# Kernel tuning notes

Measured on AMD Instinct MI355X. Metric: run time of the kernel, lower is better.

Reference implementation:

```python
import jax, jax.numpy as jnp
import numpy as np

B, H, D, V = 1024, 4, 256, 100000


def setup_inputs() -> dict:
    key = jax.random.key(0)
    k1, k2, k3, k4 = jax.random.split(key, 4)
    x = jax.random.normal(k1, (B, D), dtype=jnp.float32)
    # Glorot-normal-ish scaling for the learned matrices
    proj_mat = jax.random.normal(k2, (H * D, D), dtype=jnp.float32) * (2.0 / (H * D + D)) ** 0.5
    mix_mat = jax.random.normal(k3, (H, D), dtype=jnp.float32) * (2.0 / (H + D)) ** 0.5
    emb = jax.random.normal(k4, (V, D), dtype=jnp.float32) * 0.05
    return {"x": x, "proj_mat": proj_mat, "mix_mat": mix_mat, "emb": emb}


def reference(x, proj_mat, mix_mat, emb):
    # per-head projection: [B, H*D] -> [B, H, D]
    proj = jnp.tanh(x @ proj_mat.T).reshape(B, H, D)
    # mixture weights over heads: [B, H]
    pi = jax.nn.softmax(x @ mix_mat.T, axis=-1)
    # full-vocab logits per head: [B, H, V]
    head_logits = jnp.einsum("bhd,vd->bhv", proj, emb)
    head_probs = jax.nn.softmax(head_logits, axis=-1)
    # weighted mixture over heads -> [B, V]
    probs = jnp.einsum("bh,bhv->bv", pi, head_probs)
    return probs
```

## Files before the change

kernel.cpp:

```cpp
#include <hip/hip_runtime.h>
#include <stdint.h>


#define VOCAB 100000
#define NVB 391
#define VPAD 100096

typedef __attribute__((ext_vector_type(8))) short short8;
typedef __attribute__((ext_vector_type(4))) float f32x4;

__device__ __forceinline__ short f2bf(float f) {
  uint32_t u = __float_as_uint(f);
  u = (u + 0x7FFFu + ((u >> 16) & 1u)) >> 16;
  return (short)u;
}

#define VMCNT(n) asm volatile("s_waitcnt vmcnt(" #n ")" ::: "memory")
#define LGKM0()  asm volatile("s_waitcnt lgkmcnt(0)" ::: "memory")
#define SCHED0() __builtin_amdgcn_sched_barrier(0)
#define BAR()    __builtin_amdgcn_s_barrier()

__global__ __launch_bounds__(256) void proj_kernel(const float* __restrict__ x,
                                                   const float* __restrict__ pm,
                                                   short* __restrict__ projA) {
  __shared__ float xs[64][36];
  __shared__ float ps[64][36];
  const int tid = threadIdx.x;
  const int tx = tid & 15, ty = tid >> 4;
  const int m0 = blockIdx.y * 64, n0 = blockIdx.x * 64;
  float acc[4][4];
#pragma unroll
  for (int i = 0; i < 4; i++)
#pragma unroll
    for (int j = 0; j < 4; j++) acc[i][j] = 0.f;

  for (int k0 = 0; k0 < 256; k0 += 32) {
    const int r = tid >> 2, c = (tid & 3) * 8;
    *(float4*)&xs[r][c]     = *(const float4*)&x[(m0 + r) * 256 + k0 + c];
    *(float4*)&xs[r][c + 4] = *(const float4*)&x[(m0 + r) * 256 + k0 + c + 4];
    *(float4*)&ps[r][c]     = *(const float4*)&pm[(n0 + r) * 256 + k0 + c];
    *(float4*)&ps[r][c + 4] = *(const float4*)&pm[(n0 + r) * 256 + k0 + c + 4];
    __syncthreads();
#pragma unroll
    for (int kk = 0; kk < 32; kk += 4) {
      float4 xa[4], pb[4];
#pragma unroll
      for (int i = 0; i < 4; i++) xa[i] = *(const float4*)&xs[ty * 4 + i][kk];
#pragma unroll
      for (int j = 0; j < 4; j++) pb[j] = *(const float4*)&ps[tx * 4 + j][kk];
#pragma unroll
      for (int i = 0; i < 4; i++)
#pragma unroll
        for (int j = 0; j < 4; j++)
          acc[i][j] += xa[i].x * pb[j].x + xa[i].y * pb[j].y +
                       xa[i].z * pb[j].z + xa[i].w * pb[j].w;
    }
    __syncthreads();
  }
#pragma unroll
  for (int i = 0; i < 4; i++)
#pragma unroll
    for (int j = 0; j < 4; j++)
      projA[(size_t)(m0 + ty * 4 + i) * 1024 + (n0 + tx * 4 + j)] = f2bf(tanhf(acc[i][j]));
}

__global__ __launch_bounds__(256) void pi_kernel(const float* __restrict__ x,
                                                 const float* __restrict__ mm,
                                                 float* __restrict__ pi) {
  int b = blockIdx.x * 256 + threadIdx.x;
  if (b >= 1024) return;
  float acc[4] = {0.f, 0.f, 0.f, 0.f};
  for (int k = 0; k < 256; k += 4) {
    float4 xv = *(const float4*)&x[(size_t)b * 256 + k];
#pragma unroll
    for (int h = 0; h < 4; h++) {
      float4 mv = *(const float4*)&mm[h * 256 + k];
      acc[h] += xv.x * mv.x + xv.y * mv.y + xv.z * mv.z + xv.w * mv.w;
    }
  }
  float mx = fmaxf(fmaxf(acc[0], acc[1]), fmaxf(acc[2], acc[3]));
  float e[4], ssum = 0.f;
#pragma unroll
  for (int h = 0; h < 4; h++) { e[h] = __expf(acc[h] - mx); ssum += e[h]; }
#pragma unroll
  for (int h = 0; h < 4; h++) pi[b * 4 + h] = e[h] / ssum;
}

__global__ __launch_bounds__(256) void embB_kernel(const float* __restrict__ emb,
                                                   short* __restrict__ embB) {
  size_t i = ((size_t)blockIdx.x * 256 + threadIdx.x) * 8;
  size_t row = i >> 8;
  short8 b8;
  if (row < VOCAB) {
    float4 f0 = *(const float4*)&emb[i];
    float4 f1 = *(const float4*)&emb[i + 4];
    b8[0] = f2bf(f0.x); b8[1] = f2bf(f0.y); b8[2] = f2bf(f0.z); b8[3] = f2bf(f0.w);
    b8[4] = f2bf(f1.x); b8[5] = f2bf(f1.y); b8[6] = f2bf(f1.z); b8[7] = f2bf(f1.w);
  } else {
#pragma unroll
    for (int j = 0; j < 8; ++j) b8[j] = 0;
  }
  *(short8*)&embB[i] = b8;
}


__device__ __forceinline__ void stage_AB(const char* gA, const char* gB, char* sm,
                                         int buf, int kt, int wid) {
#pragma unroll
  for (int h = 0; h < 2; ++h)
#pragma unroll
    for (int j = 0; j < 2; ++j) {
      __builtin_amdgcn_global_load_lds(
          (const __attribute__((address_space(1))) void*)(gA + kt * 128 + h * 65536 + j * 32768),
          (__attribute__((address_space(3))) void*)(sm + buf * 65536 + h * 16384 + j * 8192 + wid * 1024),
          16, 0, 0);
      __builtin_amdgcn_global_load_lds(
          (const __attribute__((address_space(1))) void*)(gB + kt * 128 + h * 65536 + j * 32768),
          (__attribute__((address_space(3))) void*)(sm + buf * 65536 + 32768 + h * 16384 + j * 8192 + wid * 1024),
          16, 0, 0);
    }
}

template <int KT>
__device__ __forceinline__ void k_step(char* sm, const char* gA, const char* gB, int wid,
                                       f32x4 (&acc)[8][4], int aK0, int aK1, int bK0, int bK1) {
  constexpr int CB = (KT & 1) * 65536;
  if (KT < 3) {
    stage_AB(gA, gB, sm, (KT + 1) & 1, KT + 1, wid);
    SCHED0();
    VMCNT(8);
  } else {
    SCHED0();
    VMCNT(0);
  }
  BAR();
  SCHED0();

  short8 b[4][2], a0[4][2], a1[4][2];
#pragma unroll
  for (int j = 0; j < 4; ++j) {
    b[j][0] = *(const short8*)(sm + CB + bK0 + j * 2048);
    b[j][1] = *(const short8*)(sm + CB + bK1 + j * 2048);
  }
#pragma unroll
  for (int i = 0; i < 4; ++i) {
    a0[i][0] = *(const short8*)(sm + CB + aK0 + i * 2048);
    a0[i][1] = *(const short8*)(sm + CB + aK1 + i * 2048);
  }
  __builtin_amdgcn_s_setprio(1);
#pragma unroll
  for (int ks = 0; ks < 2; ++ks)
#pragma unroll
    for (int i = 0; i < 4; ++i)
#pragma unroll
      for (int j = 0; j < 4; ++j)
        acc[i][j] = __builtin_amdgcn_mfma_f32_16x16x32_bf16(a0[i][ks], b[j][ks], acc[i][j], 0, 0, 0);
  __builtin_amdgcn_s_setprio(0);
#pragma unroll
  for (int i = 0; i < 4; ++i) {
    a1[i][0] = *(const short8*)(sm + CB + aK0 + (4 + i) * 2048);
    a1[i][1] = *(const short8*)(sm + CB + aK1 + (4 + i) * 2048);
  }
  LGKM0();
  SCHED0();
  BAR();
  SCHED0();
  __builtin_amdgcn_s_setprio(1);
#pragma unroll
  for (int ks = 0; ks < 2; ++ks)
#pragma unroll
    for (int i = 0; i < 4; ++i)
#pragma unroll
      for (int j = 0; j < 4; ++j)
        acc[4 + i][j] =
            __builtin_amdgcn_mfma_f32_16x16x32_bf16(a1[i][ks], b[j][ks], acc[4 + i][j], 0, 0, 0);
  __builtin_amdgcn_s_setprio(0);
}

template <int MODE>
__global__ __launch_bounds__(512, 2) void mos_gemm8(const short* __restrict__ projA_s,
                                                    const short* __restrict__ embB_s,
                                                    const float* __restrict__ w,
                                                    float* __restrict__ part,
                                                    float* __restrict__ out) {
  __shared__ __align__(16) char sm[131072];
  const int tid = threadIdx.x;
  const int lane = tid & 63, wid = tid >> 6;
  const int wr = wid >> 2, wc = wid & 3;
  const int l15 = lane & 15, l4 = lane >> 4;

  const int id = blockIdx.x;
  const int sw = (id & 7) * 782 + (id >> 3);
  const int vb = sw >> 4, mb = sw & 15;
  const int m0 = mb * 256;
  const int v0 = vb * 256;

  const int cxor = ((tid & 7) ^ ((tid >> 3) & 7)) * 16;
  const char* gA = (const char*)projA_s + (size_t)(m0 + (tid >> 3)) * 512 + cxor;
  const char* gB = (const char*)embB_s + (size_t)(v0 + (tid >> 3)) * 512 + cxor;

  const int sA = l15 & 7;
  const int aK0 = (wr * 128 + l15) * 128 + ((l4 ^ sA) << 4);
  const int aK1 = (wr * 128 + l15) * 128 + (((4 + l4) ^ sA) << 4);
  const int bK0 = 32768 + (wc * 64 + l15) * 128 + ((l4 ^ sA) << 4);
  const int bK1 = 32768 + (wc * 64 + l15) * 128 + (((4 + l4) ^ sA) << 4);

  f32x4 acc[8][4];
#pragma unroll
  for (int i = 0; i < 8; ++i)
#pragma unroll
    for (int j = 0; j < 4; ++j) acc[i][j] = (f32x4){0.f, 0.f, 0.f, 0.f};

  stage_AB(gA, gB, sm, 0, 0, wid);
  SCHED0();

  k_step<0>(sm, gA, gB, wid, acc, aK0, aK1, bK0, bK1);
  k_step<1>(sm, gA, gB, wid, acc, aK0, aK1, bK0, bK1);
  k_step<2>(sm, gA, gB, wid, acc, aK0, aK1, bK0, bK1);
  k_step<3>(sm, gA, gB, wid, acc, aK0, aK1, bK0, bK1);

  if (MODE == 0) {
#pragma unroll
    for (int mi = 0; mi < 8; ++mi) {
      float p[4] = {0.f, 0.f, 0.f, 0.f};
#pragma unroll
      for (int ni = 0; ni < 4; ++ni) {
        int v = v0 + wc * 64 + ni * 16 + l15;
        bool ok = v < VOCAB;
#pragma unroll
        for (int r = 0; r < 4; ++r) {
          float e = __expf(acc[mi][ni][r]);
          p[r] += ok ? e : 0.f;
        }
      }
#pragma unroll
      for (int r = 0; r < 4; ++r) {
        p[r] += __shfl_xor(p[r], 1, 64);
        p[r] += __shfl_xor(p[r], 2, 64);
        p[r] += __shfl_xor(p[r], 4, 64);
        p[r] += __shfl_xor(p[r], 8, 64);
      }
      if (l15 == 0) {
        float4 pv = {p[0], p[1], p[2], p[3]};
        *(float4*)(sm + (wc * 256 + wr * 128 + mi * 16 + l4 * 4) * 4) = pv;
      }
    }
    __syncthreads();
    if (tid < 256) {
      const float* rf = (const float*)sm;
      float ssum = rf[tid] + rf[256 + tid] + rf[512 + tid] + rf[768 + tid];
      part[(size_t)vb * 4096 + m0 + tid] = ssum;
    }
  } else {
#pragma unroll
    for (int mi = 0; mi < 8; ++mi) {
      int mbase = m0 + wr * 128 + mi * 16;
      float4 wv = *(const float4*)&w[mbase + l4 * 4];
      size_t brow = (size_t)(mbase >> 2) + l4;
#pragma unroll
      for (int ni = 0; ni < 4; ++ni) {
        int v = v0 + wc * 64 + ni * 16 + l15;
        float val = wv.x * __expf(acc[mi][ni][0]) + wv.y * __expf(acc[mi][ni][1]) +
                    wv.z * __expf(acc[mi][ni][2]) + wv.w * __expf(acc[mi][ni][3]);
        if (v < VOCAB) out[brow * VOCAB + v] = val;
      }
    }
  }
}

__global__ __launch_bounds__(256) void reduce_w(const float* __restrict__ part,
                                                const float* __restrict__ pi,
                                                float* __restrict__ w) {
  int m = blockIdx.x * 256 + threadIdx.x;
  float sum = 0.f;
  for (int c = 0; c < NVB; ++c) sum += part[(size_t)c * 4096 + m];
  w[m] = pi[m] / sum;
}

extern "C" void kernel_launch(void* const* d_in, const int* in_sizes, int n_in,
                              void* d_out, int out_size, void* d_ws, size_t ws_size,
                              hipStream_t stream) {
  const float* x        = (const float*)d_in[0];
  const float* proj_mat = (const float*)d_in[1];
  const float* mix_mat  = (const float*)d_in[2];
  const float* emb      = (const float*)d_in[3];
  float* out = (float*)d_out;

  char* ws = (char*)d_ws;
  short* projA = (short*)ws;
  float* pi    = (float*)(ws + (2u << 20));
  float* w     = (float*)(ws + (2u << 20) + 16384);
  short* embB  = (short*)(ws + (4u << 20));
  float* part  = (float*)(ws + (4u << 20) + (size_t)VPAD * 512);

  dim3 g1(16, 16);
  proj_kernel<<<g1, 256, 0, stream>>>(x, proj_mat, projA);
  pi_kernel<<<4, 256, 0, stream>>>(x, mix_mat, pi);
  embB_kernel<<<VPAD / 8, 256, 0, stream>>>(emb, embB);

  mos_gemm8<0><<<16 * NVB, 512, 0, stream>>>(projA, embB, nullptr, part, nullptr);
  reduce_w<<<16, 256, 0, stream>>>(part, pi, w);
  mos_gemm8<1><<<16 * NVB, 512, 0, stream>>>(projA, embB, w, nullptr, out);
}
```

Measured before the change: 688.0 us.

## Split k-step into quarter MFMA phases interleaved with staged global-to-LDS loads

Restructures each K step of the bf16 GEMM into four MFMA quadrants, issuing next-tile A and B global_load_lds pieces between them with finer-grained vmcnt waits and barriers. The goal is to overlap memory staging with compute instead of front-loading all loads per step. It also folds log2(e) into the bf16 embedding conversion so the epilogues can use exp2f instead of __expf, saving a multiply per exponential. The extra barriers and the finer wait bookkeeping add synchronization overhead and raise the risk of ordering errors.

```diff
diff --git a/kernel.cpp b/kernel.cpp
--- a/kernel.cpp
+++ b/kernel.cpp
@@ -90,12 +90,13 @@
                                                    short* __restrict__ embB) {
   size_t i = ((size_t)blockIdx.x * 256 + threadIdx.x) * 8;
   size_t row = i >> 8;
+  const float C = 1.44269504088896f;
   short8 b8;
   if (row < VOCAB) {
     float4 f0 = *(const float4*)&emb[i];
     float4 f1 = *(const float4*)&emb[i + 4];
-    b8[0] = f2bf(f0.x); b8[1] = f2bf(f0.y); b8[2] = f2bf(f0.z); b8[3] = f2bf(f0.w);
-    b8[4] = f2bf(f1.x); b8[5] = f2bf(f1.y); b8[6] = f2bf(f1.z); b8[7] = f2bf(f1.w);
+    b8[0] = f2bf(f0.x * C); b8[1] = f2bf(f0.y * C); b8[2] = f2bf(f0.z * C); b8[3] = f2bf(f0.w * C);
+    b8[4] = f2bf(f1.x * C); b8[5] = f2bf(f1.y * C); b8[6] = f2bf(f1.z * C); b8[7] = f2bf(f1.w * C);
   } else {
 #pragma unroll
     for (int j = 0; j < 8; ++j) b8[j] = 0;
@@ -104,77 +105,91 @@
 }
 
 
-__device__ __forceinline__ void stage_AB(const char* gA, const char* gB, char* sm,
-                                         int buf, int kt, int wid) {
-#pragma unroll
-  for (int h = 0; h < 2; ++h)
-#pragma unroll
-    for (int j = 0; j < 2; ++j) {
-      __builtin_amdgcn_global_load_lds(
-          (const __attribute__((address_space(1))) void*)(gA + kt * 128 + h * 65536 + j * 32768),
-          (__attribute__((address_space(3))) void*)(sm + buf * 65536 + h * 16384 + j * 8192 + wid * 1024),
-          16, 0, 0);
-      __builtin_amdgcn_global_load_lds(
-          (const __attribute__((address_space(1))) void*)(gB + kt * 128 + h * 65536 + j * 32768),
-          (__attribute__((address_space(3))) void*)(sm + buf * 65536 + 32768 + h * 16384 + j * 8192 + wid * 1024),
-          16, 0, 0);
-    }
-}
+#define MFMA_Q(AF, BF, MOFF, NOFF)                                                        \
+  __builtin_amdgcn_s_setprio(1);                                                          \
+  _Pragma("unroll") for (int ks = 0; ks < 2; ++ks)                                        \
+      _Pragma("unroll") for (int qi = 0; qi < 4; ++qi)                                    \
+          _Pragma("unroll") for (int qj = 0; qj < 2; ++qj)                                \
+              acc[(MOFF) + qi][(NOFF) + qj] = __builtin_amdgcn_mfma_f32_16x16x32_bf16(    \
+                  AF[qi][ks], BF[qj][ks], acc[(MOFF) + qi][(NOFF) + qj], 0, 0, 0);        \
+  __builtin_amdgcn_s_setprio(0);
 
 template <int KT>
 __device__ __forceinline__ void k_step(char* sm, const char* gA, const char* gB, int wid,
                                        f32x4 (&acc)[8][4], int aK0, int aK1, int bK0, int bK1) {
-  constexpr int CB = (KT & 1) * 65536;
-  if (KT < 3) {
-    stage_AB(gA, gB, sm, (KT + 1) & 1, KT + 1, wid);
-    SCHED0();
-    VMCNT(8);
-  } else {
-    SCHED0();
-    VMCNT(0);
-  }
-  BAR();
-  SCHED0();
-
-  short8 b[4][2], a0[4][2], a1[4][2];
-#pragma unroll
-  for (int j = 0; j < 4; ++j) {
-    b[j][0] = *(const short8*)(sm + CB + bK0 + j * 2048);
-    b[j][1] = *(const short8*)(sm + CB + bK1 + j * 2048);
+  const int CB = (KT & 1) * 65536;
+  char* NB = sm + ((KT + 1) & 1) * 65536;
+  short8 a0[4][2], a1[4][2], b0[2][2], b1[2][2];
+
+#pragma unroll
+  for (int j = 0; j < 2; ++j) {
+    b0[j][0] = *(const short8*)(sm + CB + bK0 + j * 2048);
+    b0[j][1] = *(const short8*)(sm + CB + bK1 + j * 2048);
   }
 #pragma unroll
   for (int i = 0; i < 4; ++i) {
     a0[i][0] = *(const short8*)(sm + CB + aK0 + i * 2048);
     a0[i][1] = *(const short8*)(sm + CB + aK1 + i * 2048);
   }
-  __builtin_amdgcn_s_setprio(1);
-#pragma unroll
-  for (int ks = 0; ks < 2; ++ks)
-#pragma unroll
-    for (int i = 0; i < 4; ++i)
-#pragma unroll
-      for (int j = 0; j < 4; ++j)
-        acc[i][j] = __builtin_amdgcn_mfma_f32_16x16x32_bf16(a0[i][ks], b[j][ks], acc[i][j], 0, 0, 0);
-  __builtin_amdgcn_s_setprio(0);
+  if constexpr (KT < 3) {
+#pragma unroll
+    for (int h = 0; h < 2; ++h)
+      __builtin_amdgcn_global_load_lds(
+          (const __attribute__((address_space(1))) void*)(gA + (KT + 1) * 128 + h * 65536),
+          (__attribute__((address_space(3))) void*)(NB + h * 16384 + wid * 1024), 16, 0, 0);
+  }
+  SCHED0();
+  BAR();
+  LGKM0();
+  SCHED0();
+  MFMA_Q(a0, b0, 0, 0);
+  BAR();
+
+#pragma unroll
+  for (int j = 0; j < 2; ++j) {
+    b1[j][0] = *(const short8*)(sm + CB + bK0 + (2 + j) * 2048);
+    b1[j][1] = *(const short8*)(sm + CB + bK1 + (2 + j) * 2048);
+  }
+  if constexpr (KT < 3) {
+#pragma unroll
+    for (int h = 0; h < 2; ++h)
+#pragma unroll
+      for (int j = 0; j < 2; ++j)
+        __builtin_amdgcn_global_load_lds(
+            (const __attribute__((address_space(1))) void*)(gB + (KT + 1) * 128 + h * 65536 + j * 32768),
+            (__attribute__((address_space(3))) void*)(NB + 32768 + h * 16384 + j * 8192 + wid * 1024),
+            16, 0, 0);
+  }
+  SCHED0();
+  BAR();
+  LGKM0();
+  SCHED0();
+  MFMA_Q(a0, b1, 0, 2);
+  if constexpr (KT < 3) { VMCNT(6); } else { VMCNT(0); }
+  BAR();
+
 #pragma unroll
   for (int i = 0; i < 4; ++i) {
     a1[i][0] = *(const short8*)(sm + CB + aK0 + (4 + i) * 2048);
     a1[i][1] = *(const short8*)(sm + CB + aK1 + (4 + i) * 2048);
   }
+  if constexpr (KT < 3) {
+#pragma unroll
+    for (int h = 0; h < 2; ++h)
+      __builtin_amdgcn_global_load_lds(
+          (const __attribute__((address_space(1))) void*)(gA + (KT + 1) * 128 + h * 65536 + 32768),
+          (__attribute__((address_space(3))) void*)(NB + h * 16384 + 8192 + wid * 1024), 16, 0, 0);
+  }
+  SCHED0();
+  BAR();
   LGKM0();
   SCHED0();
-  BAR();
-  SCHED0();
-  __builtin_amdgcn_s_setprio(1);
-#pragma unroll
-  for (int ks = 0; ks < 2; ++ks)
-#pragma unroll
-    for (int i = 0; i < 4; ++i)
-#pragma unroll
-      for (int j = 0; j < 4; ++j)
-        acc[4 + i][j] =
-            __builtin_amdgcn_mfma_f32_16x16x32_bf16(a1[i][ks], b[j][ks], acc[4 + i][j], 0, 0, 0);
-  __builtin_amdgcn_s_setprio(0);
+  MFMA_Q(a1, b1, 4, 2);
+  BAR();
+
+  MFMA_Q(a1, b0, 4, 0);
+  if constexpr (KT < 3) { VMCNT(2); }
+  BAR();
 }
 
 template <int MODE>
@@ -211,8 +226,27 @@
 #pragma unroll
     for (int j = 0; j < 4; ++j) acc[i][j] = (f32x4){0.f, 0.f, 0.f, 0.f};
 
-  stage_AB(gA, gB, sm, 0, 0, wid);
-  SCHED0();
+#pragma unroll
+  for (int h = 0; h < 2; ++h)
+    __builtin_amdgcn_global_load_lds(
+        (const __attribute__((address_space(1))) void*)(gA + h * 65536),
+        (__attribute__((address_space(3))) void*)(sm + h * 16384 + wid * 1024), 16, 0, 0);
+#pragma unroll
+  for (int h = 0; h < 2; ++h)
+#pragma unroll
+    for (int j = 0; j < 2; ++j)
+      __builtin_amdgcn_global_load_lds(
+          (const __attribute__((address_space(1))) void*)(gB + h * 65536 + j * 32768),
+          (__attribute__((address_space(3))) void*)(sm + 32768 + h * 16384 + j * 8192 + wid * 1024),
+          16, 0, 0);
+#pragma unroll
+  for (int h = 0; h < 2; ++h)
+    __builtin_amdgcn_global_load_lds(
+        (const __attribute__((address_space(1))) void*)(gA + h * 65536 + 32768),
+        (__attribute__((address_space(3))) void*)(sm + h * 16384 + 8192 + wid * 1024), 16, 0, 0);
+  SCHED0();
+  VMCNT(2);
+  BAR();
 
   k_step<0>(sm, gA, gB, wid, acc, aK0, aK1, bK0, bK1);
   k_step<1>(sm, gA, gB, wid, acc, aK0, aK1, bK0, bK1);
@@ -229,7 +263,7 @@
         bool ok = v < VOCAB;
 #pragma unroll
         for (int r = 0; r < 4; ++r) {
-          float e = __expf(acc[mi][ni][r]);
+          float e = exp2f(acc[mi][ni][r]);
           p[r] += ok ? e : 0.f;
         }
       }
@@ -260,8 +294,8 @@
 #pragma unroll
       for (int ni = 0; ni < 4; ++ni) {
         int v = v0 + wc * 64 + ni * 16 + l15;
-        float val = wv.x * __expf(acc[mi][ni][0]) + wv.y * __expf(acc[mi][ni][1]) +
-                    wv.z * __expf(acc[mi][ni][2]) + wv.w * __expf(acc[mi][ni][3]);
+        float val = wv.x * exp2f(acc[mi][ni][0]) + wv.y * exp2f(acc[mi][ni][1]) +
+                    wv.z * exp2f(acc[mi][ni][2]) + wv.w * exp2f(acc[mi][ni][3]);
         if (v < VOCAB) out[brow * VOCAB + v] = val;
       }
     }
```

New measurement: 724.6 us. 5.3% more time.

## Keep embedding tile in registers and stream projection rows through LDS

Applied to the files above, without the earlier changes.

Restructures both GEMM passes so each 256-thread block keeps a 128-row embedding slice resident in registers across the full K=256. It then loops over 512 M rows in 64-row sub-tiles staged through a small double-buffered LDS, with the epilogue run per sub-tile. Per-strip partial sums go straight to global memory, which doubles the strip count that reduce_w sums. Out-of-range vocab stores are sent to a dump buffer instead of masked. The log2(e) factor is folded into the bf16 embedding conversion so exp2f replaces __expf. The goal is less LDS traffic and better overlap, at the cost of heavy register pressure and more partial-sum traffic.

```diff
diff --git a/kernel.cpp b/kernel.cpp
--- a/kernel.cpp
+++ b/kernel.cpp
@@ -3,7 +3,8 @@
 
 
 #define VOCAB 100000
-#define NVB 391
+#define NVB 782
+#define NSTRIPS 1564
 #define VPAD 100096
 
 typedef __attribute__((ext_vector_type(8))) short short8;
@@ -90,12 +91,13 @@
                                                    short* __restrict__ embB) {
   size_t i = ((size_t)blockIdx.x * 256 + threadIdx.x) * 8;
   size_t row = i >> 8;
+  const float C = 1.44269504088896f;
   short8 b8;
   if (row < VOCAB) {
     float4 f0 = *(const float4*)&emb[i];
     float4 f1 = *(const float4*)&emb[i + 4];
-    b8[0] = f2bf(f0.x); b8[1] = f2bf(f0.y); b8[2] = f2bf(f0.z); b8[3] = f2bf(f0.w);
-    b8[4] = f2bf(f1.x); b8[5] = f2bf(f1.y); b8[6] = f2bf(f1.z); b8[7] = f2bf(f1.w);
+    b8[0] = f2bf(f0.x * C); b8[1] = f2bf(f0.y * C); b8[2] = f2bf(f0.z * C); b8[3] = f2bf(f0.w * C);
+    b8[4] = f2bf(f1.x * C); b8[5] = f2bf(f1.y * C); b8[6] = f2bf(f1.z * C); b8[7] = f2bf(f1.w * C);
   } else {
 #pragma unroll
     for (int j = 0; j < 8; ++j) b8[j] = 0;
@@ -104,124 +106,70 @@
 }
 
 
-__device__ __forceinline__ void stage_AB(const char* gA, const char* gB, char* sm,
-                                         int buf, int kt, int wid) {
-#pragma unroll
-  for (int h = 0; h < 2; ++h)
-#pragma unroll
-    for (int j = 0; j < 2; ++j) {
+template <int VM, bool DO_STAGE, int KH>
+__device__ __forceinline__ void k_step(char* sm, const char* gA0, int sOff, int wid,
+                                       const int (&aadr)[4], const short8 (&Bf)[4][8],
+                                       f32x4 (&acc)[2][4]) {
+  constexpr int buf = KH;
+  if constexpr (DO_STAGE) {
+#pragma unroll
+    for (int j = 0; j < 4; ++j)
       __builtin_amdgcn_global_load_lds(
-          (const __attribute__((address_space(1))) void*)(gA + kt * 128 + h * 65536 + j * 32768),
-          (__attribute__((address_space(3))) void*)(sm + buf * 65536 + h * 16384 + j * 8192 + wid * 1024),
+          (const __attribute__((address_space(1))) void*)(gA0 + sOff + j * 8192),
+          (__attribute__((address_space(3))) void*)(sm + (buf ^ 1) * 16384 + j * 4096 + wid * 1024),
           16, 0, 0);
-      __builtin_amdgcn_global_load_lds(
-          (const __attribute__((address_space(1))) void*)(gB + kt * 128 + h * 65536 + j * 32768),
-          (__attribute__((address_space(3))) void*)(sm + buf * 65536 + 32768 + h * 16384 + j * 8192 + wid * 1024),
-          16, 0, 0);
-    }
-}
-
-template <int KT>
-__device__ __forceinline__ void k_step(char* sm, const char* gA, const char* gB, int wid,
-                                       f32x4 (&acc)[8][4], int aK0, int aK1, int bK0, int bK1) {
-  constexpr int CB = (KT & 1) * 65536;
-  if (KT < 3) {
-    stage_AB(gA, gB, sm, (KT + 1) & 1, KT + 1, wid);
-    SCHED0();
-    VMCNT(8);
-  } else {
-    SCHED0();
-    VMCNT(0);
-  }
+  }
+  SCHED0();
+  if constexpr (VM == 12)      { VMCNT(12); }
+  else if constexpr (VM == 6)  { VMCNT(6); }
+  else if constexpr (VM == 4)  { VMCNT(4); }
+  else                         { VMCNT(0); }
   BAR();
-  SCHED0();
-
-  short8 b[4][2], a0[4][2], a1[4][2];
-#pragma unroll
-  for (int j = 0; j < 4; ++j) {
-    b[j][0] = *(const short8*)(sm + CB + bK0 + j * 2048);
-    b[j][1] = *(const short8*)(sm + CB + bK1 + j * 2048);
-  }
-#pragma unroll
-  for (int i = 0; i < 4; ++i) {
-    a0[i][0] = *(const short8*)(sm + CB + aK0 + i * 2048);
-    a0[i][1] = *(const short8*)(sm + CB + aK1 + i * 2048);
-  }
+  short8 a[2][4];
+#pragma unroll
+  for (int mi = 0; mi < 2; ++mi)
+#pragma unroll
+    for (int ks = 0; ks < 2; ++ks)
+      a[mi][ks] = *(const short8*)(sm + buf * 16384 + mi * 4096 + aadr[ks]);
   __builtin_amdgcn_s_setprio(1);
 #pragma unroll
   for (int ks = 0; ks < 2; ++ks)
 #pragma unroll
-    for (int i = 0; i < 4; ++i)
-#pragma unroll
-      for (int j = 0; j < 4; ++j)
-        acc[i][j] = __builtin_amdgcn_mfma_f32_16x16x32_bf16(a0[i][ks], b[j][ks], acc[i][j], 0, 0, 0);
+    for (int mi = 0; mi < 2; ++mi)
+#pragma unroll
+      for (int ni = 0; ni < 4; ++ni)
+        acc[mi][ni] = __builtin_amdgcn_mfma_f32_16x16x32_bf16(a[mi][ks], Bf[ni][KH * 4 + ks],
+                                                              acc[mi][ni], 0, 0, 0);
   __builtin_amdgcn_s_setprio(0);
 #pragma unroll
-  for (int i = 0; i < 4; ++i) {
-    a1[i][0] = *(const short8*)(sm + CB + aK0 + (4 + i) * 2048);
-    a1[i][1] = *(const short8*)(sm + CB + aK1 + (4 + i) * 2048);
-  }
+  for (int mi = 0; mi < 2; ++mi)
+#pragma unroll
+    for (int ks = 2; ks < 4; ++ks)
+      a[mi][ks] = *(const short8*)(sm + buf * 16384 + mi * 4096 + aadr[ks]);
   LGKM0();
   SCHED0();
   BAR();
-  SCHED0();
   __builtin_amdgcn_s_setprio(1);
 #pragma unroll
-  for (int ks = 0; ks < 2; ++ks)
-#pragma unroll
-    for (int i = 0; i < 4; ++i)
-#pragma unroll
-      for (int j = 0; j < 4; ++j)
-        acc[4 + i][j] =
-            __builtin_amdgcn_mfma_f32_16x16x32_bf16(a1[i][ks], b[j][ks], acc[4 + i][j], 0, 0, 0);
+  for (int ks = 2; ks < 4; ++ks)
+#pragma unroll
+    for (int mi = 0; mi < 2; ++mi)
+#pragma unroll
+      for (int ni = 0; ni < 4; ++ni)
+        acc[mi][ni] = __builtin_amdgcn_mfma_f32_16x16x32_bf16(a[mi][ks], Bf[ni][KH * 4 + ks],
+                                                              acc[mi][ni], 0, 0, 0);
   __builtin_amdgcn_s_setprio(0);
 }
 
 template <int MODE>
-__global__ __launch_bounds__(512, 2) void mos_gemm8(const short* __restrict__ projA_s,
-                                                    const short* __restrict__ embB_s,
-                                                    const float* __restrict__ w,
-                                                    float* __restrict__ part,
-                                                    float* __restrict__ out) {
-  __shared__ __align__(16) char sm[131072];
-  const int tid = threadIdx.x;
-  const int lane = tid & 63, wid = tid >> 6;
-  const int wr = wid >> 2, wc = wid & 3;
-  const int l15 = lane & 15, l4 = lane >> 4;
-
-  const int id = blockIdx.x;
-  const int sw = (id & 7) * 782 + (id >> 3);
-  const int vb = sw >> 4, mb = sw & 15;
-  const int m0 = mb * 256;
-  const int v0 = vb * 256;
-
-  const int cxor = ((tid & 7) ^ ((tid >> 3) & 7)) * 16;
-  const char* gA = (const char*)projA_s + (size_t)(m0 + (tid >> 3)) * 512 + cxor;
-  const char* gB = (const char*)embB_s + (size_t)(v0 + (tid >> 3)) * 512 + cxor;
-
-  const int sA = l15 & 7;
-  const int aK0 = (wr * 128 + l15) * 128 + ((l4 ^ sA) << 4);
-  const int aK1 = (wr * 128 + l15) * 128 + (((4 + l4) ^ sA) << 4);
-  const int bK0 = 32768 + (wc * 64 + l15) * 128 + ((l4 ^ sA) << 4);
-  const int bK1 = 32768 + (wc * 64 + l15) * 128 + (((4 + l4) ^ sA) << 4);
-
-  f32x4 acc[8][4];
-#pragma unroll
-  for (int i = 0; i < 8; ++i)
-#pragma unroll
-    for (int j = 0; j < 4; ++j) acc[i][j] = (f32x4){0.f, 0.f, 0.f, 0.f};
-
-  stage_AB(gA, gB, sm, 0, 0, wid);
-  SCHED0();
-
-  k_step<0>(sm, gA, gB, wid, acc, aK0, aK1, bK0, bK1);
-  k_step<1>(sm, gA, gB, wid, acc, aK0, aK1, bK0, bK1);
-  k_step<2>(sm, gA, gB, wid, acc, aK0, aK1, bK0, bK1);
-  k_step<3>(sm, gA, gB, wid, acc, aK0, aK1, bK0, bK1);
-
+__device__ __forceinline__ void epilogue(int mt, int m0, int v0, int vb, int wr, int wc,
+                                         int l15, int l4, int tid, int bid,
+                                         const float* __restrict__ w, float* __restrict__ part,
+                                         float* __restrict__ dump, float* __restrict__ out,
+                                         f32x4 (&acc)[2][4]) {
   if (MODE == 0) {
 #pragma unroll
-    for (int mi = 0; mi < 8; ++mi) {
+    for (int mi = 0; mi < 2; ++mi) {
       float p[4] = {0.f, 0.f, 0.f, 0.f};
 #pragma unroll
       for (int ni = 0; ni < 4; ++ni) {
@@ -229,7 +177,7 @@
         bool ok = v < VOCAB;
 #pragma unroll
         for (int r = 0; r < 4; ++r) {
-          float e = __expf(acc[mi][ni][r]);
+          float e = exp2f(acc[mi][ni][r]);
           p[r] += ok ? e : 0.f;
         }
       }
@@ -241,31 +189,94 @@
         p[r] += __shfl_xor(p[r], 8, 64);
       }
       if (l15 == 0) {
+        int m = m0 + mt * 64 + wr * 32 + mi * 16 + l4 * 4;
         float4 pv = {p[0], p[1], p[2], p[3]};
-        *(float4*)(sm + (wc * 256 + wr * 128 + mi * 16 + l4 * 4) * 4) = pv;
+        *(float4*)(part + (size_t)(vb * 2 + wc) * 4096 + m) = pv;
       }
     }
-    __syncthreads();
-    if (tid < 256) {
-      const float* rf = (const float*)sm;
-      float ssum = rf[tid] + rf[256 + tid] + rf[512 + tid] + rf[768 + tid];
-      part[(size_t)vb * 4096 + m0 + tid] = ssum;
-    }
   } else {
 #pragma unroll
-    for (int mi = 0; mi < 8; ++mi) {
-      int mbase = m0 + wr * 128 + mi * 16;
+    for (int mi = 0; mi < 2; ++mi) {
+      int mbase = m0 + mt * 64 + wr * 32 + mi * 16;
       float4 wv = *(const float4*)&w[mbase + l4 * 4];
       size_t brow = (size_t)(mbase >> 2) + l4;
 #pragma unroll
       for (int ni = 0; ni < 4; ++ni) {
         int v = v0 + wc * 64 + ni * 16 + l15;
-        float val = wv.x * __expf(acc[mi][ni][0]) + wv.y * __expf(acc[mi][ni][1]) +
-                    wv.z * __expf(acc[mi][ni][2]) + wv.w * __expf(acc[mi][ni][3]);
-        if (v < VOCAB) out[brow * VOCAB + v] = val;
+        float val = wv.x * exp2f(acc[mi][ni][0]) + wv.y * exp2f(acc[mi][ni][1]) +
+                    wv.z * exp2f(acc[mi][ni][2]) + wv.w * exp2f(acc[mi][ni][3]);
+        float* tgt = (v < VOCAB) ? (out + brow * VOCAB + v)
+                                 : (dump + ((bid & 255) * 256 + tid));
+        *tgt = val;
       }
     }
   }
+#pragma unroll
+  for (int mi = 0; mi < 2; ++mi)
+#pragma unroll
+    for (int ni = 0; ni < 4; ++ni) acc[mi][ni] = (f32x4){0.f, 0.f, 0.f, 0.f};
+}
+
+template <int MODE>
+__global__ __launch_bounds__(256, 2) void mos_gemm(const short* __restrict__ projA_s,
+                                                   const short* __restrict__ embB_s,
+                                                   const float* __restrict__ w,
+                                                   float* __restrict__ part,
+                                                   float* __restrict__ dump,
+                                                   float* __restrict__ out) {
+  __shared__ __align__(16) char sm[32768];
+  const int tid = threadIdx.x;
+  const int lane = tid & 63, wid = tid >> 6;
+  const int wr = wid >> 1, wc = wid & 1;
+  const int l15 = lane & 15, l4 = lane >> 4;
+  const int bid = blockIdx.x;
+
+  const int sw = (bid & 7) * 782 + (bid >> 3);
+  const int vb = sw >> 3, me = sw & 7;
+  const int v0 = vb * 128, m0 = me * 512;
+
+  const char* gA0 = (const char*)projA_s + (size_t)(m0 + (tid >> 4)) * 512 +
+                    (((tid & 15) ^ ((tid >> 4) & 7)) << 4);
+  int aadr[4];
+#pragma unroll
+  for (int ks = 0; ks < 4; ++ks)
+    aadr[ks] = wr * 8192 + l15 * 256 + ((((ks * 4) + l4) ^ (l15 & 7)) << 4);
+
+#pragma unroll
+  for (int j = 0; j < 4; ++j)
+    __builtin_amdgcn_global_load_lds(
+        (const __attribute__((address_space(1))) void*)(gA0 + j * 8192),
+        (__attribute__((address_space(3))) void*)(sm + j * 4096 + wid * 1024), 16, 0, 0);
+  SCHED0();
+
+  short8 Bf[4][8];
+  {
+    const char* bsrc = (const char*)embB_s + (size_t)(v0 + wc * 64 + l15) * 512 + l4 * 16;
+#pragma unroll
+    for (int ni = 0; ni < 4; ++ni)
+#pragma unroll
+      for (int ks = 0; ks < 8; ++ks)
+        Bf[ni][ks] = *(const short8*)(bsrc + ni * 8192 + ks * 64);
+  }
+  SCHED0();
+
+  f32x4 acc[2][4];
+#pragma unroll
+  for (int mi = 0; mi < 2; ++mi)
+#pragma unroll
+    for (int ni = 0; ni < 4; ++ni) acc[mi][ni] = (f32x4){0.f, 0.f, 0.f, 0.f};
+
+  constexpr int VME = (MODE == 0) ? 6 : 12;
+
+#pragma unroll 1
+  for (int mt = 0; mt < 7; ++mt) {
+    k_step<VME, true, 0>(sm, gA0, mt * 32768 + 256, wid, aadr, Bf, acc);
+    k_step<4, true, 1>(sm, gA0, (mt + 1) * 32768, wid, aadr, Bf, acc);
+    epilogue<MODE>(mt, m0, v0, vb, wr, wc, l15, l4, tid, bid, w, part, dump, out, acc);
+  }
+  k_step<VME, true, 0>(sm, gA0, 7 * 32768 + 256, wid, aadr, Bf, acc);
+  k_step<0, false, 1>(sm, gA0, 0, wid, aadr, Bf, acc);
+  epilogue<MODE>(7, m0, v0, vb, wr, wc, l15, l4, tid, bid, w, part, dump, out, acc);
 }
 
 __global__ __launch_bounds__(256) void reduce_w(const float* __restrict__ part,
@@ -273,7 +284,7 @@
                                                 float* __restrict__ w) {
   int m = blockIdx.x * 256 + threadIdx.x;
   float sum = 0.f;
-  for (int c = 0; c < NVB; ++c) sum += part[(size_t)c * 4096 + m];
+  for (int c = 0; c < NSTRIPS; ++c) sum += part[(size_t)c * 4096 + m];
   w[m] = pi[m] / sum;
 }
 
@@ -292,13 +303,14 @@
   float* w     = (float*)(ws + (2u << 20) + 16384);
   short* embB  = (short*)(ws + (4u << 20));
   float* part  = (float*)(ws + (4u << 20) + (size_t)VPAD * 512);
+  float* dump  = part + (size_t)NSTRIPS * 4096;
 
   dim3 g1(16, 16);
   proj_kernel<<<g1, 256, 0, stream>>>(x, proj_mat, projA);
   pi_kernel<<<4, 256, 0, stream>>>(x, mix_mat, pi);
   embB_kernel<<<VPAD / 8, 256, 0, stream>>>(emb, embB);
 
-  mos_gemm8<0><<<16 * NVB, 512, 0, stream>>>(projA, embB, nullptr, part, nullptr);
+  mos_gemm<0><<<8 * NVB, 256, 0, stream>>>(projA, embB, nullptr, part, dump, nullptr);
   reduce_w<<<16, 256, 0, stream>>>(part, pi, w);
-  mos_gemm8<1><<<16 * NVB, 512, 0, stream>>>(projA, embB, w, nullptr, out);
-}
+  mos_gemm<1><<<8 * NVB, 256, 0, stream>>>(projA, embB, w, nullptr, dump, out);
+}
```

New measurement: 741.4 us. 7.7% more time.
